# Performance work log

Measured on AMD Instinct MI355X. Metric: run time of the kernel, lower is better.

Reference implementation:

```python
import jax, jax.numpy as jnp
import numpy as np

N = 8192
IN_F = 256
OUT_F = 256


def setup_inputs() -> dict:
    key = jax.random.key(0)
    k1, k2, k3 = jax.random.split(key, 3)
    x = jax.random.normal(k1, (N, IN_F), dtype=jnp.float32)
    adj = jax.random.randint(k2, (N, N), 0, 2, dtype=jnp.int32)
    # glorot-uniform init over last two dims of (3, 2F, O)
    stdv = float(np.sqrt(6.0 / (2 * IN_F + OUT_F)))
    weight = jax.random.uniform(k3, (3, 2 * IN_F, OUT_F), dtype=jnp.float32,
                                minval=-stdv, maxval=stdv)
    bias = jnp.zeros((OUT_F,), dtype=jnp.float32)
    return {"g": 0, "x": x, "adj": adj, "weight": weight, "bias": bias}


def reference(g, x, adj, weight, bias):
    # per-node mean over neighbors: vectorized replacement of the python loop
    mask = (adj == 1).astype(x.dtype)               # [N, N]
    deg = jnp.sum(mask, axis=1, keepdims=True)      # [N, 1]
    x1 = (mask @ x) / deg                           # [N, F] mean aggregate
    n_x = jnp.concatenate([x1, x], axis=1)          # [N, 2F]
    # [N,2F] x [3,2F,O] broadcasts to [3,N,O]
    out = jnp.einsum('nf,kfo->kno', n_x, weight) + bias
    return out
```

## Files before the change

### kernel.cpp

```cpp
#include <hip/hip_runtime.h>


typedef unsigned short u16;
typedef int   i32x4 __attribute__((ext_vector_type(4)));
typedef unsigned u32x4 __attribute__((ext_vector_type(4)));
typedef float f32x4 __attribute__((ext_vector_type(4)));

__device__ __forceinline__ u16 f2b(float f) {
  unsigned u = __builtin_bit_cast(unsigned, f);
  return (u16)((u + 0x7FFFu + ((u >> 16) & 1u)) >> 16);
}
__device__ __forceinline__ unsigned pack2(float a, float b) {
  return (unsigned)f2b(a) | ((unsigned)f2b(b) << 16);
}
__device__ __forceinline__ f32x4 mfma16(u32x4 a, u32x4 b, f32x4 c) {
  asm("v_mfma_f32_16x16x32_bf16 %0, %1, %2, %0" : "+v"(c) : "v"(a), "v"(b));
  return c;
}

__global__ __launch_bounds__(256) void prep(const float* __restrict__ x,
                                            const float* __restrict__ wgt,
                                            u16* __restrict__ xtf,
                                            u16* __restrict__ nxtf,
                                            u16* __restrict__ wtf) {
  const int b = blockIdx.x, t = threadIdx.x;
  if (b < 1024) {
    int c = b * 256 + t, kc8 = c >> 8, f = c & 255;
    const float* p = x + (size_t)kc8 * 2048 + f;
    u32x4 h;
    h.x = pack2(p[0],    p[256]);  h.y = pack2(p[512],  p[768]);
    h.z = pack2(p[1024], p[1280]); h.w = pack2(p[1536], p[1792]);
    *(u32x4*)(xtf + (size_t)c * 8) = h;
  } else if (b < 2048) {
    int c = (b - 1024) * 256 + t, kc8r = c >> 13, m = c & 8191;
    const float* p = x + (size_t)m * 256 + kc8r * 8;
    f32x4 p0 = *(const f32x4*)p, p1 = *(const f32x4*)(p + 4);
    u32x4 h;
    h.x = pack2(p0.x, p0.y); h.y = pack2(p0.z, p0.w);
    h.z = pack2(p1.x, p1.y); h.w = pack2(p1.z, p1.w);
    *(u32x4*)(nxtf + ((size_t)(32 + kc8r) * 8192 + m) * 8) = h;
  } else {
    int idx = b - 2048, kc8 = idx / 3, c = (idx % 3) * 256 + t;
    int kk = c >> 8, o = c & 255;
    const float* p = wgt + (size_t)kk * 131072 + (size_t)kc8 * 2048 + o;
    u32x4 h;
    h.x = pack2(p[0],    p[256]);  h.y = pack2(p[512],  p[768]);
    h.z = pack2(p[1024], p[1280]); h.w = pack2(p[1536], p[1792]);
    *(u32x4*)(wtf + ((size_t)kc8 * 768 + c) * 8) = h;
  }
}

__global__ __launch_bounds__(256) void phase1(const int* __restrict__ adj,
                                              const u16* __restrict__ xtf,
                                              float* __restrict__ part,
                                              int* __restrict__ degp) {
  __shared__ __align__(16) u16 As[2][32 * 72];
  __shared__ int degs[256];

  const int t = threadIdx.x, l = t & 63, w = t >> 6;
  const int l15 = l & 15, l16 = l >> 4;
  const int g = blockIdx.x & 3, mt = blockIdx.x >> 2;
  const int m0 = mt * 32, k0g = g * 2048;
  const int r = t >> 3, kq = t & 7;

  f32x4 acc[2][4] = {};
  int dsum = 0;

  const i32x4* arow = (const i32x4*)(adj + (size_t)(m0 + r) * 8192 + k0g) + kq * 2;
  const int lds_w  = r * 72 + kq * 8;
  const int lds_a0 = l15 * 72 + l16 * 8;
  const int lds_a1 = lds_a0 + 16 * 72;
  const u16* bbase = xtf + ((size_t)(k0g >> 3) + l16) * 2048 + (size_t)(w * 64 + l15) * 8;

  i32x4 p0 = __builtin_nontemporal_load(arow);
  i32x4 p1 = __builtin_nontemporal_load(arow + 1);

  for (int step = 0; step < 32; ++step) {
    dsum += p0.x + p0.y + p0.z + p0.w + p1.x + p1.y + p1.z + p1.w;
    u32x4 h;
    h.x = (p0.x ? 0x3F80u : 0u) | (p0.y ? 0x3F800000u : 0u);
    h.y = (p0.z ? 0x3F80u : 0u) | (p0.w ? 0x3F800000u : 0u);
    h.z = (p1.x ? 0x3F80u : 0u) | (p1.y ? 0x3F800000u : 0u);
    h.w = (p1.z ? 0x3F80u : 0u) | (p1.w ? 0x3F800000u : 0u);
    *(u32x4*)&As[step & 1][lds_w] = h;
    if (step < 31) {
      p0 = __builtin_nontemporal_load(arow + (step + 1) * 16);
      p1 = __builtin_nontemporal_load(arow + (step + 1) * 16 + 1);
    }
    __syncthreads();
    const u16* bs = bbase + (size_t)step * 16384;
    const u16* as_ = &As[step & 1][0];
#pragma unroll
    for (int kc = 0; kc < 2; ++kc) {
      u32x4 a0 = *(const u32x4*)(as_ + lds_a0 + kc * 32);
      u32x4 a1 = *(const u32x4*)(as_ + lds_a1 + kc * 32);
#pragma unroll
      for (int nt = 0; nt < 4; ++nt) {
        u32x4 bfr = *(const u32x4*)(bs + (size_t)kc * 8192 + nt * 128);
        acc[0][nt] = mfma16(a0, bfr, acc[0][nt]);
        acc[1][nt] = mfma16(a1, bfr, acc[1][nt]);
      }
    }
  }
  asm volatile("s_nop 7\n\ts_nop 7\n\ts_nop 7");

  degs[t] = dsum;
  __syncthreads();
  if (t < 32) {
    int s = 0;
#pragma unroll
    for (int j = 0; j < 8; ++j) s += degs[t * 8 + j];
    degp[g * 8192 + m0 + t] = s;
  }
  float* pc = part + ((size_t)g * 8192 + m0) * 256;
#pragma unroll
  for (int mt2 = 0; mt2 < 2; ++mt2)
#pragma unroll
    for (int nt = 0; nt < 4; ++nt)
#pragma unroll
      for (int i = 0; i < 4; ++i)
        pc[(size_t)(mt2 * 16 + l16 * 4 + i) * 256 + (w * 64 + nt * 16 + l15)] =
            acc[mt2][nt][i];
}

__global__ __launch_bounds__(256) void reducek(const float* __restrict__ part,
                                               const int* __restrict__ degp,
                                               u16* __restrict__ nxtf) {
  int c = blockIdx.x * 256 + threadIdx.x;
  int m = c >> 5, kc8 = c & 31;
  int deg = degp[m] + degp[8192 + m] + degp[16384 + m] + degp[24576 + m];
  float rd = 1.0f / (float)deg;
  const float* p = part + (size_t)m * 256 + kc8 * 8;
  f32x4 s0 = {}, s1 = {};
#pragma unroll
  for (int gg = 0; gg < 4; ++gg) {
    s0 += *(const f32x4*)(p + (size_t)gg * 2097152);
    s1 += *(const f32x4*)(p + (size_t)gg * 2097152 + 4);
  }
  u32x4 h;
  h.x = pack2(s0.x * rd, s0.y * rd); h.y = pack2(s0.z * rd, s0.w * rd);
  h.z = pack2(s1.x * rd, s1.y * rd); h.w = pack2(s1.z * rd, s1.w * rd);
  *(u32x4*)(nxtf + ((size_t)kc8 * 8192 + m) * 8) = h;
}

__global__ __launch_bounds__(256) void phase2(const u16* __restrict__ nxtf,
                                              const u16* __restrict__ wtf,
                                              const float* __restrict__ bias,
                                              float* __restrict__ out) {
  const int t = threadIdx.x, l = t & 63, w = t >> 6;
  const int l15 = l & 15, l16 = l >> 4;
  const int m0 = blockIdx.x * 128, c0 = blockIdx.y * 48;
  f32x4 acc[2][3] = {};
  const u16* abase = nxtf + (size_t)l16 * 65536 + (size_t)(m0 + w * 32 + l15) * 8;
  const u16* bbase = wtf  + (size_t)l16 * 6144  + (size_t)(c0 + l15) * 8;
  float bv[3];
#pragma unroll
  for (int nt = 0; nt < 3; ++nt) bv[nt] = bias[(c0 + nt * 16 + l15) & 255];
#pragma unroll 2
  for (int step = 0; step < 16; ++step) {
    u32x4 a[2], b[3];
    a[0] = *(const u32x4*)(abase + (size_t)step * 262144);
    a[1] = *(const u32x4*)(abase + (size_t)step * 262144 + 128);
#pragma unroll
    for (int nt = 0; nt < 3; ++nt)
      b[nt] = *(const u32x4*)(bbase + (size_t)step * 24576 + nt * 128);
#pragma unroll
    for (int mt2 = 0; mt2 < 2; ++mt2)
#pragma unroll
      for (int nt = 0; nt < 3; ++nt)
        acc[mt2][nt] = mfma16(a[mt2], b[nt], acc[mt2][nt]);
  }
  asm volatile("s_nop 7\n\ts_nop 7\n\ts_nop 7");
#pragma unroll
  for (int mt2 = 0; mt2 < 2; ++mt2)
#pragma unroll
    for (int nt = 0; nt < 3; ++nt) {
      int c = c0 + nt * 16 + l15;
      int kk = c >> 8, o = c & 255;
      float* op = out + (size_t)kk * 2097152 +
                  (size_t)(m0 + w * 32 + mt2 * 16 + l16 * 4) * 256 + o;
#pragma unroll
      for (int i = 0; i < 4; ++i)
        __builtin_nontemporal_store(acc[mt2][nt][i] + bv[nt], op + (size_t)i * 256);
    }
}

extern "C" void kernel_launch(void* const* d_in, const int* in_sizes, int n_in,
                              void* d_out, int out_size, void* d_ws, size_t ws_size,
                              hipStream_t stream) {
  (void)in_sizes; (void)n_in; (void)out_size; (void)ws_size;
  const float* x    = (const float*)d_in[1];
  const int*   adj  = (const int*)d_in[2];
  const float* wgt  = (const float*)d_in[3];
  const float* bias = (const float*)d_in[4];
  float* out = (float*)d_out;

  char* ws = (char*)d_ws;
  u16*   xtf  = (u16*)ws;
  u16*   nxtf = (u16*)(ws + (4ull  << 20));
  u16*   wtf  = (u16*)(ws + (12ull << 20));
  float* part = (float*)(ws + (13ull << 20));
  int*   degp = (int*)(ws + (45ull << 20));

  prep   <<<2240, 256, 0, stream>>>(x, wgt, xtf, nxtf, wtf);
  phase1 <<<1024, 256, 0, stream>>>(adj, xtf, part, degp);
  reducek<<<1024, 256, 0, stream>>>(part, degp, nxtf);
  phase2 <<<dim3(64, 16), 256, 0, stream>>>(nxtf, wtf, bias, out);
}
```

Before: 435.6 us.

## Fuse split-K reduction into phase1 with in-block K halves via LDS

Phase1 now uses 1024-thread blocks, one per 32-row tile, with two 512-thread groups each covering half of K. Their partial sums are combined in shared memory, scaled by the inverse degree and written directly as bf16 nxtf. This removes the fp32 partial buffer (32 MB written and then re-read) and the separate reducek launch. In exchange the grid drops to 256 blocks, each wave holds fewer accumulators, and there are more block-wide barriers per step, which may hurt latency hiding.

```diff
diff --git a/kernel.cpp b/kernel.cpp
--- a/kernel.cpp
+++ b/kernel.cpp
@@ -2,9 +2,10 @@
 
 
 typedef unsigned short u16;
-typedef int   i32x4 __attribute__((ext_vector_type(4)));
+typedef int      i32x4 __attribute__((ext_vector_type(4)));
+typedef unsigned u32x2 __attribute__((ext_vector_type(2)));
 typedef unsigned u32x4 __attribute__((ext_vector_type(4)));
-typedef float f32x4 __attribute__((ext_vector_type(4)));
+typedef float    f32x4 __attribute__((ext_vector_type(4)));
 
 __device__ __forceinline__ u16 f2b(float f) {
   unsigned u = __builtin_bit_cast(unsigned, f);
@@ -50,55 +51,53 @@
   }
 }
 
-__global__ __launch_bounds__(256) void phase1(const int* __restrict__ adj,
-                                              const u16* __restrict__ xtf,
-                                              float* __restrict__ part,
-                                              int* __restrict__ degp) {
-  __shared__ __align__(16) u16 As[2][32 * 72];
-  __shared__ int degs[256];
-
-  const int t = threadIdx.x, l = t & 63, w = t >> 6;
+__global__ __launch_bounds__(1024) void phase1(const int* __restrict__ adj,
+                                               const u16* __restrict__ xtf,
+                                               u16* __restrict__ nxtf) {
+  __shared__ __align__(16) u16 As[2][2][32 * 72];
+  __shared__ float Csum[32 * 260];
+  __shared__ int   degs[1024];
+  __shared__ float degrow[32];
+
+  const int t = threadIdx.x, l = t & 63;
+  const int kg = t >> 9, tg = t & 511;
+  const int wg = tg >> 6;
+  const int mf = wg >> 2, ns = wg & 3;
   const int l15 = l & 15, l16 = l >> 4;
-  const int g = blockIdx.x & 3, mt = blockIdx.x >> 2;
-  const int m0 = mt * 32, k0g = g * 2048;
-  const int r = t >> 3, kq = t & 7;
-
-  f32x4 acc[2][4] = {};
+  const int m0 = blockIdx.x * 32;
+  const int r = tg >> 4, q = tg & 15;
+
+  f32x4 acc[4] = {};
   int dsum = 0;
 
-  const i32x4* arow = (const i32x4*)(adj + (size_t)(m0 + r) * 8192 + k0g) + kq * 2;
-  const int lds_w  = r * 72 + kq * 8;
-  const int lds_a0 = l15 * 72 + l16 * 8;
-  const int lds_a1 = lds_a0 + 16 * 72;
-  const u16* bbase = xtf + ((size_t)(k0g >> 3) + l16) * 2048 + (size_t)(w * 64 + l15) * 8;
-
-  i32x4 p0 = __builtin_nontemporal_load(arow);
-  i32x4 p1 = __builtin_nontemporal_load(arow + 1);
-
-  for (int step = 0; step < 32; ++step) {
-    dsum += p0.x + p0.y + p0.z + p0.w + p1.x + p1.y + p1.z + p1.w;
-    u32x4 h;
-    h.x = (p0.x ? 0x3F80u : 0u) | (p0.y ? 0x3F800000u : 0u);
-    h.y = (p0.z ? 0x3F80u : 0u) | (p0.w ? 0x3F800000u : 0u);
-    h.z = (p1.x ? 0x3F80u : 0u) | (p1.y ? 0x3F800000u : 0u);
-    h.w = (p1.z ? 0x3F80u : 0u) | (p1.w ? 0x3F800000u : 0u);
-    *(u32x4*)&As[step & 1][lds_w] = h;
-    if (step < 31) {
-      p0 = __builtin_nontemporal_load(arow + (step + 1) * 16);
-      p1 = __builtin_nontemporal_load(arow + (step + 1) * 16 + 1);
-    }
+  const int* arow = adj + (size_t)(m0 + r) * 8192 + kg * 4096 + q * 4;
+  u16* lds_w = &As[kg][0][r * 72 + q * 4];
+  const u16* lds_a = &As[kg][0][(mf * 16 + l15) * 72 + l16 * 8];
+  const u16* bbase = xtf + ((size_t)(kg * 512 + l16) * 256 + ns * 64 + l15) * 8;
+
+  i32x4 pipe0 = __builtin_nontemporal_load((const i32x4*)arow);
+  i32x4 pipe1 = __builtin_nontemporal_load((const i32x4*)(arow + 64));
+
+  for (int step = 0; step < 64; ++step) {
+    i32x4 p = pipe0;
+    pipe0 = pipe1;
+    if (step < 62)
+      pipe1 = __builtin_nontemporal_load((const i32x4*)(arow + (step + 2) * 64));
+    dsum += p.x + p.y + p.z + p.w;
+    u32x2 h;
+    h.x = (p.x ? 0x3F80u : 0u) | (p.y ? 0x3F800000u : 0u);
+    h.y = (p.z ? 0x3F80u : 0u) | (p.w ? 0x3F800000u : 0u);
+    *(u32x2*)(lds_w + (size_t)(step & 1) * 2304) = h;
     __syncthreads();
-    const u16* bs = bbase + (size_t)step * 16384;
-    const u16* as_ = &As[step & 1][0];
+    const u16* as_ = lds_a + (size_t)(step & 1) * 2304;
+    const u16* bs  = bbase + (size_t)step * 16384;
 #pragma unroll
     for (int kc = 0; kc < 2; ++kc) {
-      u32x4 a0 = *(const u32x4*)(as_ + lds_a0 + kc * 32);
-      u32x4 a1 = *(const u32x4*)(as_ + lds_a1 + kc * 32);
+      u32x4 a = *(const u32x4*)(as_ + kc * 32);
 #pragma unroll
       for (int nt = 0; nt < 4; ++nt) {
         u32x4 bfr = *(const u32x4*)(bs + (size_t)kc * 8192 + nt * 128);
-        acc[0][nt] = mfma16(a0, bfr, acc[0][nt]);
-        acc[1][nt] = mfma16(a1, bfr, acc[1][nt]);
+        acc[nt] = mfma16(a, bfr, acc[nt]);
       }
     }
   }
@@ -109,38 +108,37 @@
   if (t < 32) {
     int s = 0;
 #pragma unroll
-    for (int j = 0; j < 8; ++j) s += degs[t * 8 + j];
-    degp[g * 8192 + m0 + t] = s;
-  }
-  float* pc = part + ((size_t)g * 8192 + m0) * 256;
-#pragma unroll
-  for (int mt2 = 0; mt2 < 2; ++mt2)
-#pragma unroll
-    for (int nt = 0; nt < 4; ++nt)
-#pragma unroll
-      for (int i = 0; i < 4; ++i)
-        pc[(size_t)(mt2 * 16 + l16 * 4 + i) * 256 + (w * 64 + nt * 16 + l15)] =
-            acc[mt2][nt][i];
-}
-
-__global__ __launch_bounds__(256) void reducek(const float* __restrict__ part,
-                                               const int* __restrict__ degp,
-                                               u16* __restrict__ nxtf) {
-  int c = blockIdx.x * 256 + threadIdx.x;
-  int m = c >> 5, kc8 = c & 31;
-  int deg = degp[m] + degp[8192 + m] + degp[16384 + m] + degp[24576 + m];
-  float rd = 1.0f / (float)deg;
-  const float* p = part + (size_t)m * 256 + kc8 * 8;
-  f32x4 s0 = {}, s1 = {};
-#pragma unroll
-  for (int gg = 0; gg < 4; ++gg) {
-    s0 += *(const f32x4*)(p + (size_t)gg * 2097152);
-    s1 += *(const f32x4*)(p + (size_t)gg * 2097152 + 4);
-  }
-  u32x4 h;
-  h.x = pack2(s0.x * rd, s0.y * rd); h.y = pack2(s0.z * rd, s0.w * rd);
-  h.z = pack2(s1.x * rd, s1.y * rd); h.w = pack2(s1.z * rd, s1.w * rd);
-  *(u32x4*)(nxtf + ((size_t)kc8 * 8192 + m) * 8) = h;
+    for (int kgg = 0; kgg < 2; ++kgg)
+#pragma unroll
+      for (int j = 0; j < 16; ++j) s += degs[kgg * 512 + t * 16 + j];
+    degrow[t] = (float)s;
+  }
+#pragma unroll
+  for (int round = 0; round < 2; ++round) {
+    if (kg == round) {
+#pragma unroll
+      for (int nt = 0; nt < 4; ++nt)
+#pragma unroll
+        for (int i = 0; i < 4; ++i) {
+          int row = mf * 16 + l16 * 4 + i;
+          int col = ns * 64 + nt * 16 + l15;
+          if (round == 0) Csum[row * 260 + col]  = acc[nt][i];
+          else            Csum[row * 260 + col] += acc[nt][i];
+        }
+    }
+    __syncthreads();
+  }
+  {
+    int rr = t & 31, kc8 = t >> 5;
+    float rd = 1.0f / degrow[rr];
+    const float* cp = &Csum[rr * 260 + kc8 * 8];
+    u32x4 h;
+    h.x = pack2(cp[0] * rd, cp[1] * rd);
+    h.y = pack2(cp[2] * rd, cp[3] * rd);
+    h.z = pack2(cp[4] * rd, cp[5] * rd);
+    h.w = pack2(cp[6] * rd, cp[7] * rd);
+    *(u32x4*)(nxtf + ((size_t)kc8 * 8192 + m0 + rr) * 8) = h;
+  }
 }
 
 __global__ __launch_bounds__(256) void phase2(const u16* __restrict__ nxtf,
@@ -196,14 +194,11 @@
   float* out = (float*)d_out;
 
   char* ws = (char*)d_ws;
-  u16*   xtf  = (u16*)ws;
-  u16*   nxtf = (u16*)(ws + (4ull  << 20));
-  u16*   wtf  = (u16*)(ws + (12ull << 20));
-  float* part = (float*)(ws + (13ull << 20));
-  int*   degp = (int*)(ws + (45ull << 20));
-
-  prep   <<<2240, 256, 0, stream>>>(x, wgt, xtf, nxtf, wtf);
-  phase1 <<<1024, 256, 0, stream>>>(adj, xtf, part, degp);
-  reducek<<<1024, 256, 0, stream>>>(part, degp, nxtf);
-  phase2 <<<dim3(64, 16), 256, 0, stream>>>(nxtf, wtf, bias, out);
-}
+  u16* xtf  = (u16*)ws;
+  u16* nxtf = (u16*)(ws + (4ull  << 20));
+  u16* wtf  = (u16*)(ws + (12ull << 20));
+
+  prep  <<<2240, 256, 0, stream>>>(x, wgt, xtf, nxtf, wtf);
+  phase1<<<256, 1024, 0, stream>>>(adj, xtf, nxtf);
+  phase2<<<dim3(64, 16), 256, 0, stream>>>(nxtf, wtf, bias, out);
+}
```

Result: slower. 481.1 us (+10.4%).

## Rewrite aggregation GEMM with 32x32 MFMA, register-shuffled adjacency, 8-way split-K

Applied to the files above, without the earlier changes.

The adjacency-times-x kernel now has each wave own a 32-row by 256-column tile using 32x32x16 bf16 MFMA. The adjacency fragments are rearranged across lanes with ds_bpermute rather than staged through shared memory, which removes the LDS writes and block barriers. Both the adjacency and x fragments are double-buffered in registers. The K dimension is split 8 ways instead of 4, giving 512 blocks, which doubles the partial-sum buffer and the work in the reduction kernel. Register pressure rises with 128 accumulator floats per lane, and each wave now reads the x tiles itself with no sharing inside the block.

```diff
diff --git a/kernel.cpp b/kernel.cpp
--- a/kernel.cpp
+++ b/kernel.cpp
@@ -2,9 +2,10 @@
 
 
 typedef unsigned short u16;
-typedef int   i32x4 __attribute__((ext_vector_type(4)));
+typedef int      i32x4 __attribute__((ext_vector_type(4)));
 typedef unsigned u32x4 __attribute__((ext_vector_type(4)));
-typedef float f32x4 __attribute__((ext_vector_type(4)));
+typedef float    f32x4 __attribute__((ext_vector_type(4)));
+typedef float    f32x16 __attribute__((ext_vector_type(16)));
 
 __device__ __forceinline__ u16 f2b(float f) {
   unsigned u = __builtin_bit_cast(unsigned, f);
@@ -15,6 +16,10 @@
 }
 __device__ __forceinline__ f32x4 mfma16(u32x4 a, u32x4 b, f32x4 c) {
   asm("v_mfma_f32_16x16x32_bf16 %0, %1, %2, %0" : "+v"(c) : "v"(a), "v"(b));
+  return c;
+}
+__device__ __forceinline__ f32x16 mfma32(u32x4 a, u32x4 b, f32x16 c) {
+  asm("v_mfma_f32_32x32x16_bf16 %0, %1, %2, %0" : "+v"(c) : "v"(a), "v"(b));
   return c;
 }
 
@@ -50,77 +55,68 @@
   }
 }
 
-__global__ __launch_bounds__(256) void phase1(const int* __restrict__ adj,
-                                              const u16* __restrict__ xtf,
-                                              float* __restrict__ part,
-                                              int* __restrict__ degp) {
-  __shared__ __align__(16) u16 As[2][32 * 72];
-  __shared__ int degs[256];
-
+__global__ __launch_bounds__(256, 2) void phase1(const int* __restrict__ adj,
+                                                 const u16* __restrict__ xtf,
+                                                 float* __restrict__ part,
+                                                 int* __restrict__ degp) {
   const int t = threadIdx.x, l = t & 63, w = t >> 6;
-  const int l15 = l & 15, l16 = l >> 4;
-  const int g = blockIdx.x & 3, mt = blockIdx.x >> 2;
-  const int m0 = mt * 32, k0g = g * 2048;
-  const int r = t >> 3, kq = t & 7;
-
-  f32x4 acc[2][4] = {};
+  const int l31 = l & 31, l32 = l >> 5;
+  const int m0 = blockIdx.x * 128 + w * 32;
+  const int k0g = blockIdx.y * 1024;
+
+  const int* abase = adj + (size_t)(m0 + (l >> 1)) * 8192 + k0g + (l & 1) * 8;
+  const int bpidx = (((l31 << 1) | l32) << 2);
+  const u16* bbase = xtf + ((size_t)((k0g >> 3) + l32) * 256 + l31) * 8;
+
+  f32x16 acc[8] = {};
   int dsum = 0;
 
-  const i32x4* arow = (const i32x4*)(adj + (size_t)(m0 + r) * 8192 + k0g) + kq * 2;
-  const int lds_w  = r * 72 + kq * 8;
-  const int lds_a0 = l15 * 72 + l16 * 8;
-  const int lds_a1 = lds_a0 + 16 * 72;
-  const u16* bbase = xtf + ((size_t)(k0g >> 3) + l16) * 2048 + (size_t)(w * 64 + l15) * 8;
-
-  i32x4 p0 = __builtin_nontemporal_load(arow);
-  i32x4 p1 = __builtin_nontemporal_load(arow + 1);
-
-  for (int step = 0; step < 32; ++step) {
+  i32x4 pa[2][2];
+  u32x4 bf[2][8];
+  pa[0][0] = __builtin_nontemporal_load((const i32x4*)abase);
+  pa[0][1] = __builtin_nontemporal_load((const i32x4*)abase + 1);
+#pragma unroll
+  for (int nt = 0; nt < 8; ++nt)
+    bf[0][nt] = *(const u32x4*)(bbase + nt * 256);
+
+#pragma unroll 2
+  for (int step = 0; step < 64; ++step) {
+    const int cur = step & 1, nxt = cur ^ 1;
+    if (step < 63) {
+      pa[nxt][0] = __builtin_nontemporal_load((const i32x4*)(abase + (step + 1) * 16));
+      pa[nxt][1] = __builtin_nontemporal_load((const i32x4*)(abase + (step + 1) * 16) + 1);
+#pragma unroll
+      for (int nt = 0; nt < 8; ++nt)
+        bf[nxt][nt] = *(const u32x4*)(bbase + (step + 1) * 4096 + nt * 256);
+    }
+    i32x4 p0 = pa[cur][0], p1 = pa[cur][1];
     dsum += p0.x + p0.y + p0.z + p0.w + p1.x + p1.y + p1.z + p1.w;
-    u32x4 h;
-    h.x = (p0.x ? 0x3F80u : 0u) | (p0.y ? 0x3F800000u : 0u);
-    h.y = (p0.z ? 0x3F80u : 0u) | (p0.w ? 0x3F800000u : 0u);
-    h.z = (p1.x ? 0x3F80u : 0u) | (p1.y ? 0x3F800000u : 0u);
-    h.w = (p1.z ? 0x3F80u : 0u) | (p1.w ? 0x3F800000u : 0u);
-    *(u32x4*)&As[step & 1][lds_w] = h;
-    if (step < 31) {
-      p0 = __builtin_nontemporal_load(arow + (step + 1) * 16);
-      p1 = __builtin_nontemporal_load(arow + (step + 1) * 16 + 1);
+    unsigned v0 = (p0.x ? 0x3F80u : 0u) | (p0.y ? 0x3F800000u : 0u);
+    unsigned v1 = (p0.z ? 0x3F80u : 0u) | (p0.w ? 0x3F800000u : 0u);
+    unsigned v2 = (p1.x ? 0x3F80u : 0u) | (p1.y ? 0x3F800000u : 0u);
+    unsigned v3 = (p1.z ? 0x3F80u : 0u) | (p1.w ? 0x3F800000u : 0u);
+    u32x4 a;
+    a.x = (unsigned)__builtin_amdgcn_ds_bpermute(bpidx, (int)v0);
+    a.y = (unsigned)__builtin_amdgcn_ds_bpermute(bpidx, (int)v1);
+    a.z = (unsigned)__builtin_amdgcn_ds_bpermute(bpidx, (int)v2);
+    a.w = (unsigned)__builtin_amdgcn_ds_bpermute(bpidx, (int)v3);
+#pragma unroll
+    for (int nt = 0; nt < 8; ++nt)
+      acc[nt] = mfma32(a, bf[cur][nt], acc[nt]);
+  }
+  asm volatile("s_nop 7\n\ts_nop 7\n\ts_nop 7");
+
+  dsum += __shfl_xor(dsum, 1);
+  if ((l & 1) == 0) degp[blockIdx.y * 8192 + m0 + (l >> 1)] = dsum;
+
+  float* pc = part + (size_t)blockIdx.y * 2097152 + (size_t)m0 * 256;
+#pragma unroll
+  for (int nt = 0; nt < 8; ++nt)
+#pragma unroll
+    for (int reg = 0; reg < 16; ++reg) {
+      int row = (reg & 3) + 8 * (reg >> 2) + 4 * l32;
+      pc[(size_t)row * 256 + nt * 32 + l31] = acc[nt][reg];
     }
-    __syncthreads();
-    const u16* bs = bbase + (size_t)step * 16384;
-    const u16* as_ = &As[step & 1][0];
-#pragma unroll
-    for (int kc = 0; kc < 2; ++kc) {
-      u32x4 a0 = *(const u32x4*)(as_ + lds_a0 + kc * 32);
-      u32x4 a1 = *(const u32x4*)(as_ + lds_a1 + kc * 32);
-#pragma unroll
-      for (int nt = 0; nt < 4; ++nt) {
-        u32x4 bfr = *(const u32x4*)(bs + (size_t)kc * 8192 + nt * 128);
-        acc[0][nt] = mfma16(a0, bfr, acc[0][nt]);
-        acc[1][nt] = mfma16(a1, bfr, acc[1][nt]);
-      }
-    }
-  }
-  asm volatile("s_nop 7\n\ts_nop 7\n\ts_nop 7");
-
-  degs[t] = dsum;
-  __syncthreads();
-  if (t < 32) {
-    int s = 0;
-#pragma unroll
-    for (int j = 0; j < 8; ++j) s += degs[t * 8 + j];
-    degp[g * 8192 + m0 + t] = s;
-  }
-  float* pc = part + ((size_t)g * 8192 + m0) * 256;
-#pragma unroll
-  for (int mt2 = 0; mt2 < 2; ++mt2)
-#pragma unroll
-    for (int nt = 0; nt < 4; ++nt)
-#pragma unroll
-      for (int i = 0; i < 4; ++i)
-        pc[(size_t)(mt2 * 16 + l16 * 4 + i) * 256 + (w * 64 + nt * 16 + l15)] =
-            acc[mt2][nt][i];
 }
 
 __global__ __launch_bounds__(256) void reducek(const float* __restrict__ part,
@@ -128,14 +124,16 @@
                                                u16* __restrict__ nxtf) {
   int c = blockIdx.x * 256 + threadIdx.x;
   int m = c >> 5, kc8 = c & 31;
-  int deg = degp[m] + degp[8192 + m] + degp[16384 + m] + degp[24576 + m];
+  int deg = 0;
+#pragma unroll
+  for (int kb = 0; kb < 8; ++kb) deg += degp[kb * 8192 + m];
   float rd = 1.0f / (float)deg;
   const float* p = part + (size_t)m * 256 + kc8 * 8;
   f32x4 s0 = {}, s1 = {};
 #pragma unroll
-  for (int gg = 0; gg < 4; ++gg) {
-    s0 += *(const f32x4*)(p + (size_t)gg * 2097152);
-    s1 += *(const f32x4*)(p + (size_t)gg * 2097152 + 4);
+  for (int kb = 0; kb < 8; ++kb) {
+    s0 += *(const f32x4*)(p + (size_t)kb * 2097152);
+    s1 += *(const f32x4*)(p + (size_t)kb * 2097152 + 4);
   }
   u32x4 h;
   h.x = pack2(s0.x * rd, s0.y * rd); h.y = pack2(s0.z * rd, s0.w * rd);
@@ -200,10 +198,10 @@
   u16*   nxtf = (u16*)(ws + (4ull  << 20));
   u16*   wtf  = (u16*)(ws + (12ull << 20));
   float* part = (float*)(ws + (13ull << 20));
-  int*   degp = (int*)(ws + (45ull << 20));
+  int*   degp = (int*)(ws + (77ull << 20));
 
   prep   <<<2240, 256, 0, stream>>>(x, wgt, xtf, nxtf, wtf);
-  phase1 <<<1024, 256, 0, stream>>>(adj, xtf, part, degp);
+  phase1 <<<dim3(64, 8), 256, 0, stream>>>(adj, xtf, part, degp);
   reducek<<<1024, 256, 0, stream>>>(part, degp, nxtf);
   phase2 <<<dim3(64, 16), 256, 0, stream>>>(nxtf, wtf, bias, out);
 }
```

After: 910.3 us. +109.0%, slower.
